# Kernel tuning notes

Hardware: AMD Instinct MI355X
Metric: run time of the kernel (lower is better)

Reference implementation:

```python
import jax, jax.numpy as jnp
import numpy as np

ACT_DIM = 2048
DICT_SIZE = 16384
K = 64
PCT_A = 0.05
PCT_B = 0.05
BATCH = 4096


def _build_masks():
    n_a = int(DICT_SIZE * PCT_A)
    n_b = int(DICT_SIZE * PCT_B)
    a_end, b_end = n_a, n_a + n_b
    enc_mask = np.ones((2, DICT_SIZE), dtype=np.float32)
    enc_mask[1, :a_end] = 0.0
    enc_mask[0, a_end:b_end] = 0.0
    dec_mask = np.ones((DICT_SIZE, 2), dtype=np.float32)
    dec_mask[:a_end, 1] = 0.0
    dec_mask[a_end:b_end, 0] = 0.0
    return jnp.asarray(enc_mask), jnp.asarray(dec_mask)


def setup_inputs() -> dict:
    key = jax.random.key(0)
    kx, ke, kd = jax.random.split(key, 3)
    enc_mask, dec_mask = _build_masks()
    x = jax.random.normal(kx, (BATCH, 2, ACT_DIM), dtype=jnp.float32)
    W_enc = jax.random.normal(ke, (2, ACT_DIM, DICT_SIZE), dtype=jnp.float32) / (ACT_DIM ** 0.5)
    W_dec = jax.random.normal(kd, (DICT_SIZE, 2, ACT_DIM), dtype=jnp.float32) / (DICT_SIZE ** 0.5)
    # _apply_masks(): zero forbidden weights at init
    W_enc = W_enc * enc_mask[:, None, :]          # (2, d, F)
    W_dec = W_dec * dec_mask[:, :, None]          # (F, 2, d)
    b_enc = jnp.zeros((DICT_SIZE,), dtype=jnp.float32)
    b_dec = jnp.zeros((2, ACT_DIM), dtype=jnp.float32)
    return {"x": x, "W_enc": W_enc, "b_enc": b_enc,
            "W_dec": W_dec, "b_dec": b_dec, "dec_mask": dec_mask}


def reference(x, W_enc, b_enc, W_dec, b_dec, dec_mask):
    # ---- encode: dense GEMM + ReLU + top-k select (no enc_mask applied) ----
    pre = jnp.einsum('bmd,mdf->bf', x, W_enc) + b_enc   # (B, F)
    pre = jax.nn.relu(pre)
    topk_vals, topk_idx = jax.lax.top_k(pre, K)          # (B, K)
    B = pre.shape[0]
    rows = jnp.arange(B)[:, None]                        # (B, 1)
    features = jnp.zeros_like(pre).at[rows, topk_idx].set(topk_vals)  # (B, F)
    # ---- decode: dec_mask enforced on decoder weights ----
    W = W_dec * dec_mask[:, :, None]                     # (F, 2, d)
    recon = jnp.einsum('bf,fmd->bmd', features, W) + b_dec  # (B, 2, d)
    return recon, features
```

## Files before the change

kernel.cpp:

```cpp
#include <hip/hip_runtime.h>
#include <stdint.h>

#define BATCH   4096
#define KDIM    4096
#define FDIM    16384
#define DDIM    4096
#define TOPK    64

typedef _Float16 half4v __attribute__((ext_vector_type(4)));
typedef _Float16 half8v __attribute__((ext_vector_type(8)));
typedef float    f32x4  __attribute__((ext_vector_type(4)));

__global__ __launch_bounds__(256) void transpose_wenc(
    const float* __restrict__ W,
    float* __restrict__ WT)
{
    __shared__ float t[64][65];
    const int nbk = KDIM / 64;
    int bk = (blockIdx.x % nbk) * 64;
    int bf = (blockIdx.x / nbk) * 64;
    int tid = threadIdx.x;
    int xx = tid & 63;
    int yy = tid >> 6;
    #pragma unroll
    for (int j = 0; j < 16; ++j) {
        int k = yy + j * 4;
        t[k][xx] = W[(size_t)(bk + k) * FDIM + bf + xx];
    }
    __syncthreads();
    #pragma unroll
    for (int j = 0; j < 16; ++j) {
        int f = yy + j * 4;
        WT[(size_t)(bf + f) * KDIM + bk + xx] = t[xx][f];
    }
}

__device__ inline ushort f2bf(float f) {
    uint32_t u = __float_as_uint(f);
    return (ushort)((u + 0x7fffu + ((u >> 16) & 1u)) >> 16);
}

__global__ __launch_bounds__(256) void wdec_to_bf16(
    const float* __restrict__ Wdec, ushort* __restrict__ Wb)
{
    const size_t total4 = (size_t)FDIM * DDIM / 4;
    size_t stride = (size_t)gridDim.x * blockDim.x;
    for (size_t i = (size_t)blockIdx.x * blockDim.x + threadIdx.x; i < total4; i += stride) {
        float4 v = *(const float4*)(Wdec + i * 4);
        ushort4 o;
        o.x = f2bf(v.x); o.y = f2bf(v.y); o.z = f2bf(v.z); o.w = f2bf(v.w);
        *(ushort4*)(Wb + i * 4) = o;
    }
}

__global__ __launch_bounds__(256) void encode_mfma_1p(
    const float* __restrict__ A,
    const float* __restrict__ B,
    const float* __restrict__ bias,
    float* __restrict__ C)
{
    __shared__ _Float16 Ah[128 * 32];
    __shared__ _Float16 Bh[128 * 32];

    int nwg = gridDim.x;
    int cpx = nwg >> 3;
    int bid = blockIdx.x;
    int wg  = (bid & 7) * cpx + (bid >> 3);

    int bm = (wg & 31) << 7;
    int bn = (wg >> 5) << 7;

    int tid  = threadIdx.x;
    int wave = tid >> 6, lane = tid & 63;
    int wr = wave >> 1, wc = wave & 1;
    int lrow = lane & 15, lgrp = lane >> 4;

    int colw = tid & 127;
    int kh   = tid >> 7;
    int nbw  = colw >> 4;
    int colb = colw & 15;

    const float* Arow = A + (size_t)bm * KDIM;

    float4 areg[4];
    float  breg[16];
    #pragma unroll
    for (int i = 0; i < 4; ++i) {
        int idx = tid + i * 256;
        areg[i] = *(const float4*)(Arow + (size_t)(idx >> 3) * KDIM + ((idx & 7) << 2));
    }
    #pragma unroll
    for (int kk = 0; kk < 16; ++kk)
        breg[kk] = B[(size_t)(kh * 16 + kk) * FDIM + bn + colw];

    f32x4 zero = {0.0f, 0.0f, 0.0f, 0.0f};
    f32x4 acc[4][4];
    #pragma unroll
    for (int mf = 0; mf < 4; ++mf)
        #pragma unroll
        for (int nf = 0; nf < 4; ++nf) acc[mf][nf] = zero;

    for (int kt = 0; kt < KDIM; kt += 32) {
        __syncthreads();

        #pragma unroll
        for (int i = 0; i < 4; ++i) {
            int idx = tid + i * 256;
            int m   = idx >> 3;
            int g   = (idx & 7) >> 1;
            int hf  = (idx & 1) << 2;
            int off = m * 32 + ((g ^ ((m >> 1) & 3)) << 3) + hf;
            float v[4] = {areg[i].x, areg[i].y, areg[i].z, areg[i].w};
            half4v h1;
            #pragma unroll
            for (int j = 0; j < 4; ++j) h1[j] = (_Float16)v[j];
            *(half4v*)&Ah[off] = h1;
        }
        {
            half8v g0h, g1h;
            #pragma unroll
            for (int kk = 0; kk < 8; ++kk) {
                g0h[kk] = (_Float16)breg[kk];
                g1h[kk] = (_Float16)breg[8 + kk];
            }
            int g0 = kh * 2, g1 = kh * 2 + 1;
            int off0 = nbw * 512 + ((colb * 4 + (g0 ^ ((colb >> 1) & 3))) << 3);
            int off1 = nbw * 512 + ((colb * 4 + (g1 ^ ((colb >> 1) & 3))) << 3);
            *(half8v*)&Bh[off0] = g0h;
            *(half8v*)&Bh[off1] = g1h;
        }
        __syncthreads();

        if (kt + 32 < KDIM) {
            #pragma unroll
            for (int i = 0; i < 4; ++i) {
                int idx = tid + i * 256;
                areg[i] = *(const float4*)(Arow + (size_t)(idx >> 3) * KDIM + kt + 32 + ((idx & 7) << 2));
            }
            #pragma unroll
            for (int kk = 0; kk < 16; ++kk)
                breg[kk] = B[(size_t)(kt + 32 + kh * 16 + kk) * FDIM + bn + colw];
        }

        half8v ahf[4], bhf[4];
        #pragma unroll
        for (int mf = 0; mf < 4; ++mf) {
            int m   = wr * 64 + mf * 16 + lrow;
            int off = m * 32 + ((lgrp ^ ((m >> 1) & 3)) << 3);
            ahf[mf] = *(half8v*)&Ah[off];
        }
        #pragma unroll
        for (int nf = 0; nf < 4; ++nf) {
            int nb  = wc * 4 + nf;
            int off = nb * 512 + ((lrow * 4 + (lgrp ^ ((lrow >> 1) & 3))) << 3);
            bhf[nf] = *(half8v*)&Bh[off];
        }

        #pragma unroll
        for (int mf = 0; mf < 4; ++mf)
            #pragma unroll
            for (int nf = 0; nf < 4; ++nf)
                acc[mf][nf] = __builtin_amdgcn_mfma_f32_16x16x32_f16(ahf[mf], bhf[nf], acc[mf][nf], 0, 0, 0);
    }

    #pragma unroll
    for (int nf = 0; nf < 4; ++nf) {
        int col = bn + wc * 64 + nf * 16 + lrow;
        float bb = bias[col];
        #pragma unroll
        for (int mf = 0; mf < 4; ++mf) {
            int row0 = bm + wr * 64 + mf * 16 + lgrp * 4;
            #pragma unroll
            for (int r = 0; r < 4; ++r) {
                float v = acc[mf][nf][r] + bb;
                C[(size_t)(row0 + r) * FDIM + col] = (v > 0.0f) ? v : 0.0f;
            }
        }
    }
}

__global__ __launch_bounds__(256) void encode_mfma(
    const float* __restrict__ A,
    const float* __restrict__ B,
    const float* __restrict__ bias,
    float* __restrict__ C)
{
    __shared__ _Float16 Ah[128 * 32];
    __shared__ _Float16 Al[128 * 32];
    __shared__ _Float16 Bh[128 * 32];

    int nwg = gridDim.x;
    int cpx = nwg >> 3;
    int bid = blockIdx.x;
    int wg  = (bid & 7) * cpx + (bid >> 3);

    int bm = (wg & 31) << 7;
    int bn = (wg >> 5) << 7;

    int tid  = threadIdx.x;
    int wave = tid >> 6, lane = tid & 63;
    int wr = wave >> 1, wc = wave & 1;
    int lrow = lane & 15, lgrp = lane >> 4;

    int colw = tid & 127;
    int kh   = tid >> 7;
    int nbw  = colw >> 4;
    int colb = colw & 15;

    const float* Arow = A + (size_t)bm * KDIM;

    float4 areg[4];
    float  breg[16];
    #pragma unroll
    for (int i = 0; i < 4; ++i) {
        int idx = tid + i * 256;
        areg[i] = *(const float4*)(Arow + (size_t)(idx >> 3) * KDIM + ((idx & 7) << 2));
    }
    #pragma unroll
    for (int kk = 0; kk < 16; ++kk)
        breg[kk] = B[(size_t)(kh * 16 + kk) * FDIM + bn + colw];

    f32x4 zero = {0.0f, 0.0f, 0.0f, 0.0f};
    f32x4 acc[4][4];
    #pragma unroll
    for (int mf = 0; mf < 4; ++mf)
        #pragma unroll
        for (int nf = 0; nf < 4; ++nf) acc[mf][nf] = zero;

    for (int kt = 0; kt < KDIM; kt += 32) {
        __syncthreads();

        #pragma unroll
        for (int i = 0; i < 4; ++i) {
            int idx = tid + i * 256;
            int m   = idx >> 3;
            int g   = (idx & 7) >> 1;
            int hf  = (idx & 1) << 2;
            int off = m * 32 + ((g ^ ((m >> 1) & 3)) << 3) + hf;
            float v[4] = {areg[i].x, areg[i].y, areg[i].z, areg[i].w};
            half4v h1, h2;
            #pragma unroll
            for (int j = 0; j < 4; ++j) {
                _Float16 h = (_Float16)v[j];
                h1[j] = h;
                h2[j] = (_Float16)(v[j] - (float)h);
            }
            *(half4v*)&Ah[off] = h1;
            *(half4v*)&Al[off] = h2;
        }
        {
            half8v g0h, g1h;
            #pragma unroll
            for (int kk = 0; kk < 8; ++kk) {
                g0h[kk] = (_Float16)breg[kk];
                g1h[kk] = (_Float16)breg[8 + kk];
            }
            int g0 = kh * 2, g1 = kh * 2 + 1;
            int off0 = nbw * 512 + ((colb * 4 + (g0 ^ ((colb >> 1) & 3))) << 3);
            int off1 = nbw * 512 + ((colb * 4 + (g1 ^ ((colb >> 1) & 3))) << 3);
            *(half8v*)&Bh[off0] = g0h;
            *(half8v*)&Bh[off1] = g1h;
        }
        __syncthreads();

        if (kt + 32 < KDIM) {
            #pragma unroll
            for (int i = 0; i < 4; ++i) {
                int idx = tid + i * 256;
                areg[i] = *(const float4*)(Arow + (size_t)(idx >> 3) * KDIM + kt + 32 + ((idx & 7) << 2));
            }
            #pragma unroll
            for (int kk = 0; kk < 16; ++kk)
                breg[kk] = B[(size_t)(kt + 32 + kh * 16 + kk) * FDIM + bn + colw];
        }

        half8v ahf[4], alf[4], bhf[4];
        #pragma unroll
        for (int mf = 0; mf < 4; ++mf) {
            int m   = wr * 64 + mf * 16 + lrow;
            int off = m * 32 + ((lgrp ^ ((m >> 1) & 3)) << 3);
            ahf[mf] = *(half8v*)&Ah[off];
            alf[mf] = *(half8v*)&Al[off];
        }
        #pragma unroll
        for (int nf = 0; nf < 4; ++nf) {
            int nb  = wc * 4 + nf;
            int off = nb * 512 + ((lrow * 4 + (lgrp ^ ((lrow >> 1) & 3))) << 3);
            bhf[nf] = *(half8v*)&Bh[off];
        }

        #pragma unroll
        for (int mf = 0; mf < 4; ++mf)
            #pragma unroll
            for (int nf = 0; nf < 4; ++nf) {
                acc[mf][nf] = __builtin_amdgcn_mfma_f32_16x16x32_f16(ahf[mf], bhf[nf], acc[mf][nf], 0, 0, 0);
                acc[mf][nf] = __builtin_amdgcn_mfma_f32_16x16x32_f16(alf[mf], bhf[nf], acc[mf][nf], 0, 0, 0);
            }
    }

    #pragma unroll
    for (int nf = 0; nf < 4; ++nf) {
        int col = bn + wc * 64 + nf * 16 + lrow;
        float bb = bias[col];
        #pragma unroll
        for (int mf = 0; mf < 4; ++mf) {
            int row0 = bm + wr * 64 + mf * 16 + lgrp * 4;
            #pragma unroll
            for (int r = 0; r < 4; ++r) {
                float v = acc[mf][nf][r] + bb;
                C[(size_t)(row0 + r) * FDIM + col] = (v > 0.0f) ? v : 0.0f;
            }
        }
    }
}

#define MAXCAND  32
#define LISTCAP  96

__global__ __launch_bounds__(512) void topk_decode(
    float* __restrict__ feat,
    const float* __restrict__ x,
    const float* __restrict__ Wenc,
    const float* __restrict__ WencT,
    const float* __restrict__ benc,
    const float* __restrict__ Wdec,
    const ushort* __restrict__ Wb,
    const float* __restrict__ bdec,
    const float* __restrict__ dmask,
    float* __restrict__ recon,
    float eps)
{
    int b   = blockIdx.x;
    int tid = threadIdx.x;
    int wv  = tid >> 6;
    int lane = tid & 63;
    float* frow = feat + (size_t)b * FDIM;

    float r[32];
    #pragma unroll
    for (int i = 0; i < 32; ++i) r[i] = frow[tid + i * 512];

    __shared__ uint32_t hist[8][256];
    __shared__ uint32_t scan[256];
    __shared__ uint32_t sh_prefix, sh_rem;
    __shared__ int   s_ncand, s_ndef, s_n;
    __shared__ int   s_cidx[MAXCAND];
    __shared__ float s_cval[MAXCAND];
    __shared__ int   s_sel[MAXCAND];
    __shared__ int   L_idx[LISTCAP];
    __shared__ float L_v0[LISTCAP], L_v1[LISTCAP];
    __shared__ double s_exact[MAXCAND];

    if (tid == 0) { s_ncand = 0; s_ndef = 0; s_n = 0; }

    #pragma unroll
    for (int i = 0; i < 4; ++i) ((uint32_t*)hist)[tid + i * 512] = 0u;
    __syncthreads();
    #pragma unroll
    for (int i = 0; i < 32; ++i) {
        uint32_t u = __float_as_uint(r[i]);
        if (u) atomicAdd(&hist[wv][u >> 24], 1u);
    }
    __syncthreads();
    if (tid < 256) {
        int rb = 255 - tid;
        uint32_t s = 0;
        #pragma unroll
        for (int w = 0; w < 8; ++w) s += hist[w][rb];
        scan[tid] = s;
    }
    __syncthreads();
    #pragma unroll
    for (int ofs = 1; ofs < 256; ofs <<= 1) {
        uint32_t tv = 0;
        if (tid < 256 && tid >= ofs) tv = scan[tid - ofs];
        __syncthreads();
        if (tid < 256) scan[tid] += tv;
        __syncthreads();
    }
    bool small = (scan[255] <= TOPK);

    uint32_t prefix = 0, rem = TOPK;
    if (!small) {
        if (tid < 256) {
            uint32_t cum  = scan[tid];
            uint32_t prev = (tid == 0) ? 0u : scan[tid - 1];
            if (cum >= rem && prev < rem) {
                sh_prefix = (uint32_t)(255 - tid);
                sh_rem    = rem - prev;
            }
        }
        __syncthreads();
        prefix = sh_prefix;
        rem    = sh_rem;
        __syncthreads();

        for (int byt = 2; byt >= 0; --byt) {
            #pragma unroll
            for (int i = 0; i < 4; ++i) ((uint32_t*)hist)[tid + i * 512] = 0u;
            __syncthreads();
            int shift_hi = (byt + 1) * 8;
            #pragma unroll
            for (int i = 0; i < 32; ++i) {
                uint32_t u = __float_as_uint(r[i]);
                if ((u >> shift_hi) == prefix)
                    atomicAdd(&hist[wv][(u >> (byt * 8)) & 255u], 1u);
            }
            __syncthreads();
            if (tid < 256) {
                int rb = 255 - tid;
                uint32_t s = 0;
                #pragma unroll
                for (int w = 0; w < 8; ++w) s += hist[w][rb];
                scan[tid] = s;
            }
            __syncthreads();
            #pragma unroll
            for (int ofs = 1; ofs < 256; ofs <<= 1) {
                uint32_t tv = 0;
                if (tid < 256 && tid >= ofs) tv = scan[tid - ofs];
                __syncthreads();
                if (tid < 256) scan[tid] += tv;
                __syncthreads();
            }
            if (tid < 256) {
                uint32_t cum  = scan[tid];
                uint32_t prev = (tid == 0) ? 0u : scan[tid - 1];
                if (cum >= rem && prev < rem) {
                    sh_prefix = (prefix << 8) | (uint32_t)(255 - tid);
                    sh_rem    = rem - prev;
                }
            }
            __syncthreads();
            prefix = sh_prefix;
            rem    = sh_rem;
            __syncthreads();
        }

        float T  = __uint_as_float(prefix);
        float hi = T + eps;
        float lo = T - eps;

        int mydef = 0;
        #pragma unroll
        for (int i = 0; i < 32; ++i) {
            float val = r[i];
            int   f   = tid + i * 512;
            if (val > hi) {
                ++mydef;
                int s = atomicAdd(&s_n, 1);
                if (s < LISTCAP) {
                    L_idx[s] = f;
                    L_v0[s]  = val * dmask[2 * f + 0];
                    L_v1[s]  = val * dmask[2 * f + 1];
                }
            } else if (val >= lo && val > 0.0f) {
                int s = atomicAdd(&s_ncand, 1);
                if (s < MAXCAND) { s_cidx[s] = f; s_cval[s] = val; }
                r[i] = 0.0f;
            } else {
                r[i] = 0.0f;
            }
        }
        atomicAdd(&s_ndef, mydef);
        #pragma unroll
        for (int i = 0; i < 32; ++i) frow[tid + i * 512] = r[i];
        __syncthreads();

        int A    = (s_ncand < MAXCAND) ? s_ncand : MAXCAND;
        int need = TOPK - s_ndef;

        if (A > need) {
            const float* xr = x + (size_t)b * KDIM;
            if (WencT != nullptr) {
                const float4* x4 = (const float4*)xr;
                for (int c0 = 0; c0 < A; c0 += 8) {
                    int c = c0 + wv;
                    if (c < A) {
                        int f = s_cidx[c];
                        const float4* wt = (const float4*)(WencT + (size_t)f * KDIM);
                        double s = 0.0;
                        #pragma unroll
                        for (int i = 0; i < 16; ++i) {
                            float4 wv4 = wt[lane + i * 64];
                            float4 xv4 = x4[lane + i * 64];
                            s += (double)xv4.x * (double)wv4.x + (double)xv4.y * (double)wv4.y
                               + (double)xv4.z * (double)wv4.z + (double)xv4.w * (double)wv4.w;
                        }
                        #pragma unroll
                        for (int ofs = 32; ofs > 0; ofs >>= 1)
                            s += __shfl_down(s, ofs, 64);
                        if (lane == 0) s_exact[c] = s + (double)benc[f];
                    }
                }
            } else {
                for (int c0 = 0; c0 < A; c0 += 8) {
                    int c = c0 + wv;
                    if (c < A) {
                        int f = s_cidx[c];
                        double s = 0.0;
                        #pragma unroll 8
                        for (int i = 0; i < 64; ++i) {
                            int k = lane + i * 64;
                            s += (double)xr[k] * (double)Wenc[(size_t)k * FDIM + f];
                        }
                        #pragma unroll
                        for (int ofs = 32; ofs > 0; ofs >>= 1)
                            s += __shfl_down(s, ofs, 64);
                        if (lane == 0) s_exact[c] = s + (double)benc[f];
                    }
                }
            }
            __syncthreads();
            if (tid == 0) {
                for (int c = 0; c < A; ++c) s_sel[c] = 0;
                for (int rr = 0; rr < need; ++rr) {
                    int best = -1;
                    for (int c = 0; c < A; ++c) {
                        if (s_sel[c]) continue;
                        if (best < 0 || s_exact[c] > s_exact[best] ||
                            (s_exact[c] == s_exact[best] && s_cidx[c] < s_cidx[best]))
                            best = c;
                    }
                    if (best >= 0) s_sel[best] = 1;
                }
            }
        } else {
            if (tid == 0)
                for (int c = 0; c < A; ++c) s_sel[c] = 1;
        }
        __syncthreads();

        if (tid < A && s_sel[tid]) {
            int   f   = s_cidx[tid];
            float val = s_cval[tid];
            frow[f] = val;
            int s = atomicAdd(&s_n, 1);
            if (s < LISTCAP) {
                L_idx[s] = f;
                L_v0[s]  = val * dmask[2 * f + 0];
                L_v1[s]  = val * dmask[2 * f + 1];
            }
        }
        __syncthreads();
    } else {
        #pragma unroll
        for (int i = 0; i < 32; ++i) {
            float val = r[i];
            if (val != 0.0f) {
                int f = tid + i * 512;
                int s = atomicAdd(&s_n, 1);
                if (s < LISTCAP) {
                    L_idx[s] = f;
                    L_v0[s]  = val * dmask[2 * f + 0];
                    L_v1[s]  = val * dmask[2 * f + 1];
                }
            }
        }
        __syncthreads();
    }

    int n = (s_n < LISTCAP) ? s_n : LISTCAP;

    const float4* b4 = (const float4*)bdec;
    float4 a0 = b4[tid];
    float4 a1 = b4[tid + 512];

    if (Wb != nullptr) {
        #pragma unroll 4
        for (int t = 0; t < n; ++t) {
            int f = L_idx[t];
            float s0 = L_v0[t], s1 = L_v1[t];
            const ushort4* w = (const ushort4*)(Wb + (size_t)f * DDIM);
            ushort4 u0 = w[tid];
            ushort4 u1 = w[tid + 512];
            a0.x = fmaf(s0, __uint_as_float((uint32_t)u0.x << 16), a0.x);
            a0.y = fmaf(s0, __uint_as_float((uint32_t)u0.y << 16), a0.y);
            a0.z = fmaf(s0, __uint_as_float((uint32_t)u0.z << 16), a0.z);
            a0.w = fmaf(s0, __uint_as_float((uint32_t)u0.w << 16), a0.w);
            a1.x = fmaf(s1, __uint_as_float((uint32_t)u1.x << 16), a1.x);
            a1.y = fmaf(s1, __uint_as_float((uint32_t)u1.y << 16), a1.y);
            a1.z = fmaf(s1, __uint_as_float((uint32_t)u1.z << 16), a1.z);
            a1.w = fmaf(s1, __uint_as_float((uint32_t)u1.w << 16), a1.w);
        }
    } else {
        #pragma unroll 4
        for (int t = 0; t < n; ++t) {
            int f = L_idx[t];
            float s0 = L_v0[t], s1 = L_v1[t];
            const float4* w = (const float4*)(Wdec + (size_t)f * DDIM);
            float4 w0 = w[tid];
            float4 w1 = w[tid + 512];
            a0.x = fmaf(s0, w0.x, a0.x); a0.y = fmaf(s0, w0.y, a0.y);
            a0.z = fmaf(s0, w0.z, a0.z); a0.w = fmaf(s0, w0.w, a0.w);
            a1.x = fmaf(s1, w1.x, a1.x); a1.y = fmaf(s1, w1.y, a1.y);
            a1.z = fmaf(s1, w1.z, a1.z); a1.w = fmaf(s1, w1.w, a1.w);
        }
    }

    float4* out = (float4*)(recon + (size_t)b * DDIM);
    out[tid]       = a0;
    out[tid + 512] = a1;
}

extern "C" void kernel_launch(void* const* d_in, const int* in_sizes, int n_in,
                              void* d_out, int out_size, void* d_ws, size_t ws_size,
                              hipStream_t stream)
{
    const float* x     = (const float*)d_in[0];
    const float* Wenc  = (const float*)d_in[1];
    const float* benc  = (const float*)d_in[2];
    const float* Wdec  = (const float*)d_in[3];
    const float* bdec  = (const float*)d_in[4];
    const float* dmask = (const float*)d_in[5];

    float* recon = (float*)d_out;
    float* feat  = recon + (size_t)BATCH * DDIM;

    const size_t MB = 1024 * 1024;
    bool wt    = (ws_size >= 256 * MB);
    bool wball = (ws_size >= 384 * MB);

    char* wsb = (char*)d_ws;
    float* WencT = wt ? (float*)wsb : nullptr;
    ushort* Wb = nullptr;
    if (wball)                         Wb = (ushort*)(wsb + 256 * MB);
    else if (!wt && ws_size >= 128*MB) Wb = (ushort*)wsb;

    if (wt)
        transpose_wenc<<<dim3((KDIM / 64) * (FDIM / 64)), 256, 0, stream>>>(Wenc, WencT);
    if (Wb)
        wdec_to_bf16<<<dim3(2048), 256, 0, stream>>>(Wdec, Wb);

    float eps;
    if (wt) {
        eps = 1e-2f;
        encode_mfma_1p<<<dim3((BATCH / 128) * (FDIM / 128)), 256, 0, stream>>>(x, Wenc, benc, feat);
    } else {
        eps = 5e-3f;
        encode_mfma<<<dim3((BATCH / 128) * (FDIM / 128)), 256, 0, stream>>>(x, Wenc, benc, feat);
    }

    topk_decode<<<dim3(BATCH), 512, 0, stream>>>(feat, x, Wenc, WencT, benc,
                                                 Wdec, Wb, bdec, dmask, recon, eps);
}
```

Measured before the change: 2.283 ms.

## Read transposed encoder weights with vector loads and double the K tile to 64

The encode GEMM now reads the already-transposed W_enc (WencT) so each thread loads contiguous float4 rows instead of 16 strided scalar loads per tile. The K tile grows from 32 to 64, which halves the number of barrier pairs, and the shared-memory swizzle is adjusted to the 64-wide layout. This raises register pressure (16 float4 prefetch registers per thread) and doubles LDS use per block.

```diff
diff --git a/kernel.cpp b/kernel.cpp
--- a/kernel.cpp
+++ b/kernel.cpp
@@ -53,14 +53,14 @@
     }
 }
 
-__global__ __launch_bounds__(256) void encode_mfma_1p(
+__global__ __launch_bounds__(256) void encode_mfma_1p_bt(
     const float* __restrict__ A,
-    const float* __restrict__ B,
+    const float* __restrict__ BT,
     const float* __restrict__ bias,
     float* __restrict__ C)
 {
-    __shared__ _Float16 Ah[128 * 32];
-    __shared__ _Float16 Bh[128 * 32];
+    __shared__ _Float16 Ah[128 * 64];
+    __shared__ _Float16 Bh[128 * 64];
 
     int nwg = gridDim.x;
     int cpx = nwg >> 3;
@@ -81,17 +81,17 @@
     int colb = colw & 15;
 
     const float* Arow = A + (size_t)bm * KDIM;
-
-    float4 areg[4];
-    float  breg[16];
-    #pragma unroll
-    for (int i = 0; i < 4; ++i) {
+    const float* Brow = BT + (size_t)(bn + colw) * KDIM + kh * 32;
+
+    float4 areg[8], breg[8];
+    #pragma unroll
+    for (int i = 0; i < 8; ++i) {
         int idx = tid + i * 256;
-        areg[i] = *(const float4*)(Arow + (size_t)(idx >> 3) * KDIM + ((idx & 7) << 2));
-    }
-    #pragma unroll
-    for (int kk = 0; kk < 16; ++kk)
-        breg[kk] = B[(size_t)(kh * 16 + kk) * FDIM + bn + colw];
+        areg[i] = *(const float4*)(Arow + (size_t)(idx >> 4) * KDIM + ((idx & 15) << 2));
+    }
+    #pragma unroll
+    for (int j = 0; j < 8; ++j)
+        breg[j] = *(const float4*)(Brow + j * 4);
 
     f32x4 zero = {0.0f, 0.0f, 0.0f, 0.0f};
     f32x4 acc[4][4];
@@ -100,67 +100,71 @@
         #pragma unroll
         for (int nf = 0; nf < 4; ++nf) acc[mf][nf] = zero;
 
-    for (int kt = 0; kt < KDIM; kt += 32) {
-        __syncthreads();
-
-        #pragma unroll
-        for (int i = 0; i < 4; ++i) {
+    for (int kt = 0; kt < KDIM; kt += 64) {
+        __syncthreads();
+
+        #pragma unroll
+        for (int i = 0; i < 8; ++i) {
             int idx = tid + i * 256;
-            int m   = idx >> 3;
-            int g   = (idx & 7) >> 1;
-            int hf  = (idx & 1) << 2;
-            int off = m * 32 + ((g ^ ((m >> 1) & 3)) << 3) + hf;
-            float v[4] = {areg[i].x, areg[i].y, areg[i].z, areg[i].w};
-            half4v h1;
-            #pragma unroll
-            for (int j = 0; j < 4; ++j) h1[j] = (_Float16)v[j];
-            *(half4v*)&Ah[off] = h1;
-        }
-        {
-            half8v g0h, g1h;
-            #pragma unroll
-            for (int kk = 0; kk < 8; ++kk) {
-                g0h[kk] = (_Float16)breg[kk];
-                g1h[kk] = (_Float16)breg[8 + kk];
-            }
-            int g0 = kh * 2, g1 = kh * 2 + 1;
-            int off0 = nbw * 512 + ((colb * 4 + (g0 ^ ((colb >> 1) & 3))) << 3);
-            int off1 = nbw * 512 + ((colb * 4 + (g1 ^ ((colb >> 1) & 3))) << 3);
-            *(half8v*)&Bh[off0] = g0h;
-            *(half8v*)&Bh[off1] = g1h;
-        }
-        __syncthreads();
-
-        if (kt + 32 < KDIM) {
-            #pragma unroll
-            for (int i = 0; i < 4; ++i) {
+            int m   = idx >> 4;
+            int q   = idx & 15;
+            int g   = q >> 1;
+            int hf  = (q & 1) << 2;
+            int off = m * 64 + ((g ^ (m & 7)) << 3) + hf;
+            half4v h;
+            h[0] = (_Float16)areg[i].x; h[1] = (_Float16)areg[i].y;
+            h[2] = (_Float16)areg[i].z; h[3] = (_Float16)areg[i].w;
+            *(half4v*)&Ah[off] = h;
+        }
+        #pragma unroll
+        for (int c2 = 0; c2 < 4; ++c2) {
+            half8v g8;
+            float4 v0 = breg[c2 * 2], v1 = breg[c2 * 2 + 1];
+            g8[0] = (_Float16)v0.x; g8[1] = (_Float16)v0.y;
+            g8[2] = (_Float16)v0.z; g8[3] = (_Float16)v0.w;
+            g8[4] = (_Float16)v1.x; g8[5] = (_Float16)v1.y;
+            g8[6] = (_Float16)v1.z; g8[7] = (_Float16)v1.w;
+            int c  = kh * 4 + c2;
+            int cp = c ^ (colb & 7);
+            int off = nbw * 1024 + colb * 64 + cp * 8;
+            *(half8v*)&Bh[off] = g8;
+        }
+        __syncthreads();
+
+        if (kt + 64 < KDIM) {
+            #pragma unroll
+            for (int i = 0; i < 8; ++i) {
                 int idx = tid + i * 256;
-                areg[i] = *(const float4*)(Arow + (size_t)(idx >> 3) * KDIM + kt + 32 + ((idx & 7) << 2));
-            }
-            #pragma unroll
-            for (int kk = 0; kk < 16; ++kk)
-                breg[kk] = B[(size_t)(kt + 32 + kh * 16 + kk) * FDIM + bn + colw];
-        }
-
-        half8v ahf[4], bhf[4];
-        #pragma unroll
-        for (int mf = 0; mf < 4; ++mf) {
-            int m   = wr * 64 + mf * 16 + lrow;
-            int off = m * 32 + ((lgrp ^ ((m >> 1) & 3)) << 3);
-            ahf[mf] = *(half8v*)&Ah[off];
-        }
-        #pragma unroll
-        for (int nf = 0; nf < 4; ++nf) {
-            int nb  = wc * 4 + nf;
-            int off = nb * 512 + ((lrow * 4 + (lgrp ^ ((lrow >> 1) & 3))) << 3);
-            bhf[nf] = *(half8v*)&Bh[off];
-        }
-
-        #pragma unroll
-        for (int mf = 0; mf < 4; ++mf)
-            #pragma unroll
-            for (int nf = 0; nf < 4; ++nf)
-                acc[mf][nf] = __builtin_amdgcn_mfma_f32_16x16x32_f16(ahf[mf], bhf[nf], acc[mf][nf], 0, 0, 0);
+                areg[i] = *(const float4*)(Arow + (size_t)(idx >> 4) * KDIM + kt + 64 + ((idx & 15) << 2));
+            }
+            #pragma unroll
+            for (int j = 0; j < 8; ++j)
+                breg[j] = *(const float4*)(Brow + kt + 64 + j * 4);
+        }
+
+        #pragma unroll
+        for (int kk = 0; kk < 2; ++kk) {
+            half8v ahf[4], bhf[4];
+            #pragma unroll
+            for (int mf = 0; mf < 4; ++mf) {
+                int m   = wr * 64 + mf * 16 + lrow;
+                int g   = kk * 4 + lgrp;
+                int off = m * 64 + ((g ^ (m & 7)) << 3);
+                ahf[mf] = *(half8v*)&Ah[off];
+            }
+            #pragma unroll
+            for (int nf = 0; nf < 4; ++nf) {
+                int nb  = wc * 4 + nf;
+                int cp  = (kk * 4 + lgrp) ^ (lrow & 7);
+                int off = nb * 1024 + lrow * 64 + cp * 8;
+                bhf[nf] = *(half8v*)&Bh[off];
+            }
+            #pragma unroll
+            for (int mf = 0; mf < 4; ++mf)
+                #pragma unroll
+                for (int nf = 0; nf < 4; ++nf)
+                    acc[mf][nf] = __builtin_amdgcn_mfma_f32_16x16x32_f16(ahf[mf], bhf[nf], acc[mf][nf], 0, 0, 0);
+        }
     }
 
     #pragma unroll
@@ -635,7 +639,7 @@
     float eps;
     if (wt) {
         eps = 1e-2f;
-        encode_mfma_1p<<<dim3((BATCH / 128) * (FDIM / 128)), 256, 0, stream>>>(x, Wenc, benc, feat);
+        encode_mfma_1p_bt<<<dim3((BATCH / 128) * (FDIM / 128)), 256, 0, stream>>>(x, WencT, benc, feat);
     } else {
         eps = 5e-3f;
         encode_mfma<<<dim3((BATCH / 128) * (FDIM / 128)), 256, 0, stream>>>(x, Wenc, benc, feat);
```

Result: slower. 3.019 ms (+32.2%).
